# Kernel optimization log

Hardware: AMD Instinct MI355X
Metric: run time of the kernel (lower is better)

The kernel has to match this reference:

```python
import jax, jax.numpy as jnp
import numpy as np

K = 50          # NEC paper uses p=50 neighbors
DELTA = 1e-3    # kernel smoothing constant


def setup_inputs() -> dict:
    key = jax.random.key(0)
    ks = jax.random.split(key, 8)
    B, D_IN, D, A, C = 512, 2, 128, 3, 200000
    s = lambda fan_in: 1.0 / np.sqrt(fan_in)
    return {
        "x": jax.random.normal(ks[0], (B, D_IN), jnp.float32),
        "W1": jax.random.normal(ks[1], (D_IN, D), jnp.float32) * s(D_IN),
        "b1": jnp.zeros((D,), jnp.float32),
        "W2": jax.random.normal(ks[2], (D, D), jnp.float32) * s(D),
        "b2": jnp.zeros((D,), jnp.float32),
        "W3": jax.random.normal(ks[3], (D, D), jnp.float32) * s(D),
        "b3": jnp.zeros((D,), jnp.float32),
        "W4": jax.random.normal(ks[4], (D, D), jnp.float32) * s(D),
        "b4": jnp.zeros((D,), jnp.float32),
        "keys": jax.random.normal(ks[5], (A, C, D), jnp.float32),
        "mem_values": jax.random.normal(ks[6], (A, C), jnp.float32),
    }


def _encode(x, W1, b1, W2, b2, W3, b3, W4, b4):
    h = jax.nn.relu(x @ W1 + b1)
    h = jax.nn.relu(h @ W2 + b2)
    h = jax.nn.relu(h @ W3 + b3)
    return h @ W4 + b4  # [B, D]


def _dnd_lookup(h, keys, mem_values):
    # h: [B, D]; keys: [A, C, D]; mem_values: [A, C]
    q2 = jnp.sum(h * h, axis=-1)                       # [B]
    k2 = jnp.sum(keys * keys, axis=-1)                 # [A, C]
    cross = jnp.einsum("bd,acd->bac", h, keys)         # [B, A, C]
    d2 = jnp.maximum(q2[:, None, None] + k2[None] - 2.0 * cross, 0.0)
    neg_d, idx = jax.lax.top_k(-d2, K)                  # [B, A, K]
    d_top = -neg_d
    w = 1.0 / (d_top + DELTA)                           # NEC kernel
    w = w / jnp.sum(w, axis=-1, keepdims=True)
    a_idx = jnp.arange(keys.shape[0])[None, :, None]    # [1, A, 1]
    v_top = mem_values[a_idx, idx]                      # gather -> [B, A, K]
    values = jnp.sum(w * v_top, axis=-1)                # [B, A]
    return values


def reference(x, W1, b1, W2, b2, W3, b3, W4, b4, keys, mem_values):
    h = _encode(x, W1, b1, W2, b2, W3, b3, W4, b4)
    values = _dnd_lookup(h, keys, mem_values)
    actions = jnp.argmax(values, axis=-1)
    return values, actions
```

## Files before the change

### kernel.cpp

```cpp
#include <hip/hip_runtime.h>
#include <hip/hip_bf16.h>
#include <math.h>

#define B_    512
#define DIM   128
#define A_    3
#define C_    200000
#define K_    50
#define DELTA 1e-3

typedef __attribute__((ext_vector_type(8))) short bf16x8;
typedef __attribute__((ext_vector_type(4))) float f32x4;

#define NBIN_A 128
#define CAP_A  1024
#define ROWCH  12500

#define NSEG3  32
#define TPS3   98
#define NT3    3125

#define AOFF_H64   0u
#define AOFF_H32   524288u
#define AOFF_HBF   786432u
#define AOFF_Q2    917504u
#define AOFF_V64   1718272u
#define AOFF_BINS  8022016u
#define NEED_A     (8022016ull + 307200000ull)

#define NBIN_B 192
#define CAP_B  768
#define BM_B   64
#define BN_B   128
#define TPC_B  16
#define CHUNK_B (TPC_B*BN_B)
#define NCH_B  ((C_ + CHUNK_B - 1)/CHUNK_B)

#define BOFF_H32   0u
#define BOFF_H64   262144u
#define BOFF_Q2    786432u
#define BOFF_K2    788480u
#define BOFF_HIST  3188480u
#define BOFF_TAU   4368128u
#define BOFF_CNT   4374272u
#define BOFF_V64   4380416u
#define BOFF_CAND  4392704u

static __device__ inline unsigned short f2bf(float x) {
    union { float f; unsigned u; } c; c.f = x;
    unsigned r = (c.u + 0x7FFFu + ((c.u >> 16) & 1u)) >> 16;
    return (unsigned short)r;
}
static __device__ inline unsigned pkbf(float a, float b) {
    __hip_bfloat162 t = __float22bfloat162_rn(make_float2(a, b));
    union { __hip_bfloat162 h; unsigned u; } cv; cv.h = t; return cv.u;
}

__global__ __launch_bounds__(128) void mlp_kernel(
    const float* __restrict__ x,
    const float* __restrict__ W1, const float* __restrict__ b1,
    const float* __restrict__ W2, const float* __restrict__ b2,
    const float* __restrict__ W3, const float* __restrict__ b3,
    const float* __restrict__ W4, const float* __restrict__ b4,
    float* __restrict__ h32, unsigned short* __restrict__ hbf,
    double* __restrict__ h64, float* __restrict__ q2)
{
    int b = blockIdx.x, t = threadIdx.x;
    __shared__ double s0[DIM], s1[DIM];
    double x0 = (double)x[b*2+0], x1 = (double)x[b*2+1];
    double h = x0*(double)W1[t] + x1*(double)W1[DIM+t] + (double)b1[t];
    s0[t] = h > 0.0 ? h : 0.0;
    __syncthreads();
    double acc = (double)b2[t];
    for (int k = 0; k < DIM; k++) acc += s0[k]*(double)W2[k*DIM+t];
    s1[t] = acc > 0.0 ? acc : 0.0;
    __syncthreads();
    acc = (double)b3[t];
    for (int k = 0; k < DIM; k++) acc += s1[k]*(double)W3[k*DIM+t];
    s0[t] = acc > 0.0 ? acc : 0.0;
    __syncthreads();
    acc = (double)b4[t];
    for (int k = 0; k < DIM; k++) acc += s0[k]*(double)W4[k*DIM+t];
    h64[b*DIM+t] = acc;
    float hf = (float)acc;
    h32[b*DIM+t] = hf;
    hbf[b*DIM+t] = f2bf(hf);
    s1[t] = acc*acc;
    __syncthreads();
    for (int s = 64; s > 0; s >>= 1) { if (t < s) s1[t] += s1[t+s]; __syncthreads(); }
    if (t == 0) q2[b] = (float)s1[0];
}

static __device__ inline void load4(float4 lv[4], const float* __restrict__ ka,
                                    int nrow, int hh) {
    const float4* gp = (const float4*)(ka + (size_t)nrow*DIM) + hh*4;
    #pragma unroll
    for (int qq = 0; qq < 4; qq++) lv[qq] = gp[qq];
}
static __device__ inline void conv_store(const float4 lv[4], char* sBn,
                                         float* k2n, int r, int hh) {
    float ss = 0.f;
    int4 pk0, pk1;
    {
        float4 v0 = lv[0], v1 = lv[1];
        ss += v0.x*v0.x + v0.y*v0.y + v0.z*v0.z + v0.w*v0.w
            + v1.x*v1.x + v1.y*v1.y + v1.z*v1.z + v1.w*v1.w;
        pk0.x = (int)pkbf(v0.x, v0.y); pk0.y = (int)pkbf(v0.z, v0.w);
        pk0.z = (int)pkbf(v1.x, v1.y); pk0.w = (int)pkbf(v1.z, v1.w);
    }
    {
        float4 v0 = lv[2], v1 = lv[3];
        ss += v0.x*v0.x + v0.y*v0.y + v0.z*v0.z + v0.w*v0.w
            + v1.x*v1.x + v1.y*v1.y + v1.z*v1.z + v1.w*v1.w;
        pk1.x = (int)pkbf(v0.x, v0.y); pk1.y = (int)pkbf(v0.z, v0.w);
        pk1.z = (int)pkbf(v1.x, v1.y); pk1.w = (int)pkbf(v1.z, v1.w);
    }
    char* base = sBn + r*256;
    *(int4*)(base + (((hh*2    ) ^ (r & 7)) << 4)) = pk0;
    *(int4*)(base + (((hh*2 + 1) ^ (r & 7)) << 4)) = pk1;
    ss += __shfl_xor(ss, 1, 64);
    ss += __shfl_xor(ss, 2, 64);
    ss += __shfl_xor(ss, 4, 64);
    if (hh == 0) k2n[r] = ss;
}

__global__ __launch_bounds__(512, 6) void gemm3_kernel(
    const float* __restrict__ keys, const unsigned short* __restrict__ hbf,
    const float* __restrict__ q2, unsigned char* __restrict__ bins)
{
    const int seg = blockIdx.x, my = blockIdx.y, a = blockIdx.z;
    const int b0 = my*64;
    const int tid = threadIdx.x;
    const int lane = tid & 63, w = tid >> 6;
    const int lm = lane & 15, kh = lane >> 4;
    const int wn = w & 1, wm = w >> 1;

    const int tbeg = seg*TPS3;
    int tcnt = NT3 - tbeg;
    if (tcnt <= 0) return;
    if (tcnt > TPS3) tcnt = TPS3;

    __shared__ __align__(16) short sA[8192];
    __shared__ __align__(16) short sB[2][8192];
    __shared__ float q2s[64];
    __shared__ float k2s[2][64];

    {
        #pragma unroll
        for (int u = 0; u < 2; u++) {
            int idx = tid*2 + u;
            int rr = idx >> 4, cc = idx & 15;
            const int4 gv = ((const int4*)hbf)[(size_t)(b0 + rr)*16 + cc];
            *(int4*)((char*)sA + rr*256 + ((cc ^ (rr & 7)) << 4)) = gv;
        }
        if (tid < 64) q2s[tid] = q2[b0 + tid];
    }

    const int r = tid >> 3, hh = tid & 7;
    const float* ka = keys + (size_t)a*C_*DIM;

    float4 lv[4];
    load4(lv, ka, tbeg*64 + r, hh);
    conv_store(lv, (char*)&sB[0][0], k2s[0], r, hh);
    __syncthreads();

    unsigned char* bp_base = bins + ((size_t)(a*B_ + b0))*C_;
    const int bcol = wm*16 + lm;
    const size_t soff0 = (size_t)bcol*C_ + (wn*32 + 0*16 + kh*4);
    const size_t soff1 = (size_t)bcol*C_ + (wn*32 + 1*16 + kh*4);

    unsigned pk_prev0 = 0, pk_prev1 = 0;
    int n0_prev = 0;

    int cur = 0;
    for (int t = 0; t < tcnt; t++) {
        const int n0 = (tbeg + t)*64;
        const bool more = (t + 1 < tcnt);

        if (more) load4(lv, ka, n0 + 64 + r, hh);
        if (t > 0) {
            *(unsigned*)(bp_base + n0_prev + soff0) = pk_prev0;
            *(unsigned*)(bp_base + n0_prev + soff1) = pk_prev1;
        }

        f32x4 acc[2];
        acc[0] = (f32x4){0.f, 0.f, 0.f, 0.f};
        acc[1] = (f32x4){0.f, 0.f, 0.f, 0.f};

        const char* sBc = (const char*)&sB[cur][0];
        #pragma unroll
        for (int kst = 0; kst < 4; kst++) {
            bf16x8 af[2], bfv;
            #pragma unroll
            for (int i = 0; i < 2; i++) {
                int nr = wn*32 + i*16 + lm;
                af[i] = *(const bf16x8*)(sBc + nr*256 + ((((kst<<2) + kh) ^ (nr & 7)) << 4));
            }
            {
                int br = wm*16 + lm;
                bfv = *(const bf16x8*)((const char*)sA + br*256 + ((((kst<<2) + kh) ^ (br & 7)) << 4));
            }
            #pragma unroll
            for (int i = 0; i < 2; i++)
                acc[i] = __builtin_amdgcn_mfma_f32_16x16x32_bf16(af[i], bfv, acc[i], 0, 0, 0);
        }

        {
            const float q2v = q2s[bcol];
            #pragma unroll
            for (int i = 0; i < 2; i++) {
                int nl = wn*32 + i*16 + kh*4;
                float4 kq = *(const float4*)&k2s[cur][nl];
                unsigned pk = 0;
                #pragma unroll
                for (int rg = 0; rg < 4; rg++) {
                    float kv = (rg == 0) ? kq.x : (rg == 1) ? kq.y : (rg == 2) ? kq.z : kq.w;
                    float d2v = (q2v + kv) - 2.0f*acc[i][rg];
                    float dc = fminf(fmaxf(d2v, 16.0f), 4095.0f);
                    unsigned bin = (__float_as_uint(dc) >> 19) - 2096u;
                    pk |= bin << (8*rg);
                }
                if (i == 0) pk_prev0 = pk; else pk_prev1 = pk;
            }
            n0_prev = n0;
        }

        if (more) conv_store(lv, (char*)&sB[cur ^ 1][0], k2s[cur ^ 1], r, hh);
        __syncthreads();
        cur ^= 1;
    }
    *(unsigned*)(bp_base + n0_prev + soff0) = pk_prev0;
    *(unsigned*)(bp_base + n0_prev + soff1) = pk_prev1;
}

__global__ __launch_bounds__(512) void finish_kernel(
    const unsigned char* __restrict__ bins, const float* __restrict__ keys,
    const double* __restrict__ h64, const float* __restrict__ mem_values,
    float* __restrict__ out_values, double* __restrict__ val64)
{
    const int q = blockIdx.x;
    const int a = q >> 9, b = q & 511;
    const int p = b*A_ + a;
    const int tid = threadIdx.x;

    __shared__ unsigned hist_s[NBIN_A*32];
    __shared__ unsigned hc[NBIN_A];
    __shared__ double hd[DIM];
    __shared__ int    cidx[CAP_A];
    __shared__ double d2s[CAP_A];
    __shared__ float  vs[CAP_A];
    __shared__ double redv[8];
    __shared__ int    redi8[8];
    __shared__ double acc_w, acc_wv;
    __shared__ unsigned cnt_s;
    __shared__ int thr_s;

    for (int i = tid; i < NBIN_A*32; i += 512) hist_s[i] = 0;
    for (int i = tid; i < DIM; i += 512) hd[i] = h64[(size_t)b*DIM + i];
    if (tid == 0) { cnt_s = 0; acc_w = 0.0; acc_wv = 0.0; }
    __syncthreads();

    const uint4* row = (const uint4*)(bins + (size_t)q*C_);
    const int rep = tid & 31;
    for (int ch = tid; ch < ROWCH; ch += 512) {
        uint4 v = row[ch];
        unsigned d[4] = {v.x, v.y, v.z, v.w};
        #pragma unroll
        for (int e = 0; e < 4; e++) {
            unsigned x = d[e];
            atomicAdd(&hist_s[((x      ) & 127u)*32 + rep], 1u);
            atomicAdd(&hist_s[((x >>  8) & 127u)*32 + rep], 1u);
            atomicAdd(&hist_s[((x >> 16) & 127u)*32 + rep], 1u);
            atomicAdd(&hist_s[((x >> 24) & 127u)*32 + rep], 1u);
        }
    }
    __syncthreads();
    if (tid < NBIN_A) {
        unsigned s = 0;
        #pragma unroll
        for (int r2 = 0; r2 < 32; r2++) s += hist_s[tid*32 + r2];
        hc[tid] = s;
    }
    __syncthreads();
    if (tid == 0) {
        unsigned cum = 0; int jsel = NBIN_A-1;
        for (int j = 0; j < NBIN_A; j++) { cum += hc[j]; if (cum >= K_) { jsel = j; break; } }
        unsigned c1 = cum + (jsel+1 < NBIN_A ? hc[jsel+1] : 0u);
        unsigned c2 = c1  + (jsel+2 < NBIN_A ? hc[jsel+2] : 0u);
        int jt = (c2 <= 768u) ? jsel+2 : jsel+1;
        if (jt > NBIN_A-1) jt = NBIN_A-1;
        thr_s = jt + 1;
    }
    __syncthreads();
    const unsigned thr  = (unsigned)thr_s;
    const unsigned addv = (128u - thr) * 0x01010101u;
    for (int ch = tid; ch < ROWCH; ch += 512) {
        uint4 v = row[ch];
        unsigned d[4] = {v.x, v.y, v.z, v.w};
        #pragma unroll
        for (int e = 0; e < 4; e++) {
            unsigned m = (d[e] + addv) & 0x80808080u;
            if (m != 0x80808080u) {
                #pragma unroll
                for (int by = 0; by < 4; by++) {
                    if (!((m >> (8*by + 7)) & 1u)) {
                        unsigned pos = atomicAdd(&cnt_s, 1u);
                        if (pos < CAP_A) cidx[pos] = ch*16 + e*4 + by;
                    }
                }
            }
        }
    }
    __syncthreads();
    int n = (int)cnt_s; if (n > CAP_A) n = CAP_A;

    for (int i = tid; i < n; i += 512) {
        int c = cidx[i];
        const float4* kr = (const float4*)(keys + ((size_t)a*C_ + c)*DIM);
        double s0 = 0.0, s1 = 0.0;
        #pragma unroll 4
        for (int kq = 0; kq < 32; kq++) {
            float4 kv = kr[kq];
            double d0 = hd[4*kq+0] - (double)kv.x;
            double d1 = hd[4*kq+1] - (double)kv.y;
            double d2 = hd[4*kq+2] - (double)kv.z;
            double d3 = hd[4*kq+3] - (double)kv.w;
            s0 += d0*d0 + d1*d1; s1 += d2*d2 + d3*d3;
        }
        d2s[i] = s0 + s1;
        vs[i]  = mem_values[(size_t)a*C_ + c];
    }
    __syncthreads();

    int kk = n < K_ ? n : K_;
    for (int t = 0; t < kk; t++) {
        double best = 1e300; int bi = -1;
        for (int i = tid; i < n; i += 512)
            if (d2s[i] < best) { best = d2s[i]; bi = i; }
        #pragma unroll
        for (int off = 32; off > 0; off >>= 1) {
            double ov = __shfl_xor(best, off, 64);
            int    oi = __shfl_xor(bi,   off, 64);
            if (ov < best) { best = ov; bi = oi; }
        }
        int wv = tid >> 6;
        if ((tid & 63) == 0) { redv[wv] = best; redi8[wv] = bi; }
        __syncthreads();
        if (tid == 0) {
            double bv = redv[0]; int wi = redi8[0];
            #pragma unroll
            for (int u = 1; u < 8; u++)
                if (redv[u] < bv) { bv = redv[u]; wi = redi8[u]; }
            double d = d2s[wi]; if (d < 0.0) d = 0.0;
            double wgt = 1.0 / (d + DELTA);
            acc_w += wgt; acc_wv += wgt * (double)vs[wi];
            d2s[wi] = 2e300;
        }
        __syncthreads();
    }
    if (tid == 0) {
        double v = acc_wv / acc_w;
        out_values[p] = (float)v;
        val64[p] = v;
    }
}

__global__ __launch_bounds__(256) void k2_kernel(const float* __restrict__ keys,
                                                 float* __restrict__ k2)
{
    int r = blockIdx.x*4 + (threadIdx.x >> 6);
    int lane = threadIdx.x & 63;
    float2 v = ((const float2*)keys)[(size_t)r*64 + lane];
    float s = v.x*v.x + v.y*v.y;
    #pragma unroll
    for (int off = 32; off > 0; off >>= 1) s += __shfl_down(s, off, 64);
    if (lane == 0) k2[r] = s;
}

template<int MODE>
__global__ __launch_bounds__(256) void pass_kernel(
    const float* __restrict__ keys, const float* __restrict__ h32,
    const float* __restrict__ q2,   const float* __restrict__ k2,
    unsigned* __restrict__ hist,    const float* __restrict__ tau,
    unsigned* __restrict__ cnt,     int* __restrict__ cand)
{
    const int bt = blockIdx.x;
    const int ch = blockIdx.y;
    const int a  = blockIdx.z;
    const int b0 = bt*BM_B;
    const int tid = threadIdx.x;
    const int tx = tid & 31, ty = tid >> 5;

    __shared__ float4 hs4[BM_B*33];
    __shared__ float4 ks4[BN_B*33];
    __shared__ float  q2s[BM_B];
    __shared__ float  taus[BM_B];
    __shared__ unsigned hist_s[MODE == 0 ? BM_B*NBIN_B : 1];

    #pragma unroll
    for (int q = 0; q < BM_B*32/256; q++) {
        int flat = q*256 + tid; int row = flat >> 5, kq = flat & 31;
        hs4[row*33 + kq] = ((const float4*)h32)[(size_t)(b0+row)*32 + kq];
    }
    if (tid < BM_B) {
        q2s[tid] = q2[b0+tid];
        if (MODE == 1) taus[tid] = tau[(b0+tid)*A_ + a];
    }
    if (MODE == 0) for (int i = tid; i < BM_B*NBIN_B; i += 256) hist_s[i] = 0;
    const float* __restrict__ k2g = k2 + (size_t)a*C_;

    for (int t = 0; t < TPC_B; t++) {
        int n0 = ch*CHUNK_B + t*BN_B;
        if (n0 >= C_) break;
        __syncthreads();
        #pragma unroll
        for (int q = 0; q < 16; q++) {
            int flat = q*256 + tid; int row = flat >> 5, kq = flat & 31;
            int nr = n0 + row; if (nr >= C_) nr = C_-1;
            ks4[row*33 + kq] = ((const float4*)keys)[((size_t)a*C_ + nr)*32 + kq];
        }
        __syncthreads();

        float acc[8][4];
        #pragma unroll
        for (int i = 0; i < 8; i++)
            #pragma unroll
            for (int j = 0; j < 4; j++) acc[i][j] = 0.0f;

        for (int kq = 0; kq < 32; kq++) {
            float4 hv[8], kv[4];
            #pragma unroll
            for (int i = 0; i < 8; i++) hv[i] = hs4[(ty*8+i)*33 + kq];
            #pragma unroll
            for (int j = 0; j < 4; j++) kv[j] = ks4[(j*32+tx)*33 + kq];
            #pragma unroll
            for (int i = 0; i < 8; i++)
                #pragma unroll
                for (int j = 0; j < 4; j++)
                    acc[i][j] += hv[i].x*kv[j].x + hv[i].y*kv[j].y
                               + hv[i].z*kv[j].z + hv[i].w*kv[j].w;
        }

        #pragma unroll
        for (int i = 0; i < 8; i++) {
            int bl = ty*8 + i;
            float q2b = q2s[bl];
            #pragma unroll
            for (int j = 0; j < 4; j++) {
                int n = n0 + j*32 + tx;
                if (n < C_) {
                    float d2f = fmaxf(q2b + k2g[n] - 2.0f*acc[i][j], 0.0f);
                    if (MODE == 0) {
                        int bin = (int)(__float_as_uint(d2f + 1.0f) >> 19) - 2032;
                        bin = bin < 0 ? 0 : (bin > NBIN_B-1 ? NBIN_B-1 : bin);
                        atomicAdd(&hist_s[bl*NBIN_B + bin], 1u);
                    } else {
                        if (d2f < taus[bl]) {
                            int p = (b0+bl)*A_ + a;
                            unsigned pos = atomicAdd(&cnt[p], 1u);
                            if (pos < CAP_B) cand[(size_t)p*CAP_B + pos] = n;
                        }
                    }
                }
            }
        }
    }
    if (MODE == 0) {
        __syncthreads();
        for (int i = tid; i < BM_B*NBIN_B; i += 256) {
            unsigned v = hist_s[i];
            if (v) {
                int bl = i / NBIN_B, bin = i % NBIN_B;
                atomicAdd(&hist[(size_t)((b0+bl)*A_ + a)*NBIN_B + bin], v);
            }
        }
    }
}

__global__ __launch_bounds__(256) void tauB_kernel(const unsigned* __restrict__ hist,
                                                   float* __restrict__ tau)
{
    int p = blockIdx.x*256 + threadIdx.x;
    if (p >= B_*A_) return;
    const unsigned* hp = hist + (size_t)p*NBIN_B;
    unsigned cum = 0; int jsel = NBIN_B-1;
    for (int j = 0; j < NBIN_B; j++) { cum += hp[j]; if (cum >= K_) { jsel = j; break; } }
    tau[p] = __uint_as_float((unsigned)(2034 + jsel) << 19) - 1.0f;
}

__global__ __launch_bounds__(256) void select_kernel(
    const float* __restrict__ keys, const double* __restrict__ h64,
    const float* __restrict__ mem_values,
    const unsigned* __restrict__ cnt, const int* __restrict__ cand,
    float* __restrict__ out_values, double* __restrict__ val64, int cap)
{
    int p = blockIdx.x; int b = p / A_, a = p % A_;
    int tid = threadIdx.x;
    __shared__ double hd[DIM];
    __shared__ double d2s[CAP_A];
    __shared__ float  vs[CAP_A];
    __shared__ double redv[4];
    __shared__ int    redi4[4];
    __shared__ double acc_w, acc_wv;

    for (int i = tid; i < DIM; i += 256) hd[i] = h64[(size_t)b*DIM + i];
    if (tid == 0) { acc_w = 0.0; acc_wv = 0.0; }
    __syncthreads();

    int n = (int)cnt[p]; if (n > cap) n = cap;
    for (int i = tid; i < n; i += 256) {
        int c = cand[(size_t)p*cap + i];
        const float4* kr = (const float4*)(keys + ((size_t)a*C_ + c)*DIM);
        double s0 = 0.0, s1 = 0.0;
        #pragma unroll 4
        for (int kq = 0; kq < 32; kq++) {
            float4 kv = kr[kq];
            double d0 = hd[4*kq+0] - (double)kv.x;
            double d1 = hd[4*kq+1] - (double)kv.y;
            double d2 = hd[4*kq+2] - (double)kv.z;
            double d3 = hd[4*kq+3] - (double)kv.w;
            s0 += d0*d0 + d1*d1; s1 += d2*d2 + d3*d3;
        }
        d2s[i] = s0 + s1;
        vs[i]  = mem_values[(size_t)a*C_ + c];
    }
    __syncthreads();

    int kk = n < K_ ? n : K_;
    for (int t = 0; t < kk; t++) {
        double best = 1e300; int bi = -1;
        for (int i = tid; i < n; i += 256)
            if (d2s[i] < best) { best = d2s[i]; bi = i; }
        #pragma unroll
        for (int off = 32; off > 0; off >>= 1) {
            double ov = __shfl_xor(best, off, 64);
            int    oi = __shfl_xor(bi,   off, 64);
            if (ov < best) { best = ov; bi = oi; }
        }
        int wv = tid >> 6;
        if ((tid & 63) == 0) { redv[wv] = best; redi4[wv] = bi; }
        __syncthreads();
        if (tid == 0) {
            double bv = redv[0]; int wi = redi4[0];
            if (redv[1] < bv) { bv = redv[1]; wi = redi4[1]; }
            if (redv[2] < bv) { bv = redv[2]; wi = redi4[2]; }
            if (redv[3] < bv) { bv = redv[3]; wi = redi4[3]; }
            double d = d2s[wi]; if (d < 0.0) d = 0.0;
            double wgt = 1.0 / (d + DELTA);
            acc_w += wgt; acc_wv += wgt * (double)vs[wi];
            d2s[wi] = 2e300;
        }
        __syncthreads();
    }
    if (tid == 0) {
        double v = acc_wv / acc_w;
        out_values[p] = (float)v;
        val64[p] = v;
    }
}

__global__ void argmax_kernel(const double* __restrict__ val64, float* __restrict__ out)
{
    int b = blockIdx.x*blockDim.x + threadIdx.x;
    if (b >= B_) return;
    double v0 = val64[b*A_+0], v1 = val64[b*A_+1], v2 = val64[b*A_+2];
    int bi = 0; double bv = v0;
    if (v1 > bv) { bv = v1; bi = 1; }
    if (v2 > bv) { bv = v2; bi = 2; }
    out[B_*A_ + b] = (float)bi;
}

extern "C" void kernel_launch(void* const* d_in, const int* in_sizes, int n_in,
                              void* d_out, int out_size, void* d_ws, size_t ws_size,
                              hipStream_t stream)
{
    const float* x    = (const float*)d_in[0];
    const float* W1   = (const float*)d_in[1];
    const float* b1   = (const float*)d_in[2];
    const float* W2   = (const float*)d_in[3];
    const float* b2   = (const float*)d_in[4];
    const float* W3   = (const float*)d_in[5];
    const float* b3   = (const float*)d_in[6];
    const float* W4   = (const float*)d_in[7];
    const float* b4   = (const float*)d_in[8];
    const float* keys = (const float*)d_in[9];
    const float* memv = (const float*)d_in[10];

    char* ws = (char*)d_ws;

    if (ws_size >= NEED_A) {
        double*         h64  = (double*)        (ws + AOFF_H64);
        float*          h32  = (float*)         (ws + AOFF_H32);
        unsigned short* hbf  = (unsigned short*)(ws + AOFF_HBF);
        float*          q2   = (float*)         (ws + AOFF_Q2);
        double*         v64  = (double*)        (ws + AOFF_V64);
        unsigned char*  bins = (unsigned char*) (ws + AOFF_BINS);

        mlp_kernel<<<B_, 128, 0, stream>>>(x, W1, b1, W2, b2, W3, b3, W4, b4, h32, hbf, h64, q2);
        gemm3_kernel<<<dim3(NSEG3, 8, A_), 512, 0, stream>>>(keys, hbf, q2, bins);
        finish_kernel<<<B_*A_, 512, 0, stream>>>(bins, keys, h64, memv, (float*)d_out, v64);
        argmax_kernel<<<2, 256, 0, stream>>>(v64, (float*)d_out);
    } else {
        float*          h32  = (float*)         (ws + BOFF_H32);
        double*         h64  = (double*)        (ws + BOFF_H64);
        float*          q2   = (float*)         (ws + BOFF_Q2);
        float*          k2   = (float*)         (ws + BOFF_K2);
        unsigned*       hist = (unsigned*)      (ws + BOFF_HIST);
        float*          tau  = (float*)         (ws + BOFF_TAU);
        unsigned*       cnt  = (unsigned*)      (ws + BOFF_CNT);
        double*         v64  = (double*)        (ws + BOFF_V64);
        int*            cand = (int*)           (ws + BOFF_CAND);
        unsigned short* hbf  = (unsigned short*)(ws + BOFF_CAND);

        hipMemsetAsync(ws + BOFF_HIST, 0, (BOFF_CNT + B_*A_*4) - BOFF_HIST, stream);

        mlp_kernel<<<B_, 128, 0, stream>>>(x, W1, b1, W2, b2, W3, b3, W4, b4, h32, hbf, h64, q2);
        k2_kernel<<<(A_*C_)/4, 256, 0, stream>>>(keys, k2);
        pass_kernel<0><<<dim3(B_/BM_B, NCH_B, A_), 256, 0, stream>>>(keys, h32, q2, k2, hist, nullptr, nullptr, nullptr);
        tauB_kernel<<<(B_*A_ + 255)/256, 256, 0, stream>>>(hist, tau);
        pass_kernel<1><<<dim3(B_/BM_B, NCH_B, A_), 256, 0, stream>>>(keys, h32, q2, k2, nullptr, tau, cnt, cand);
        select_kernel<<<B_*A_, 256, 0, stream>>>(keys, h64, memv, cnt, cand, (float*)d_out, v64, CAP_B);
        argmax_kernel<<<2, 256, 0, stream>>>(v64, (float*)d_out);
    }
}
```

Before: 1.085 ms.

## Keep all queries resident in LDS so each key tile is read once

```diff
diff --git a/kernel.cpp b/kernel.cpp
--- a/kernel.cpp
+++ b/kernel.cpp
@@ -16,9 +16,9 @@
 #define CAP_A  1024
 #define ROWCH  12500
 
-#define NSEG3  32
-#define TPS3   98
-#define NT3    3125
+#define NBLK4  250
+#define GT4    32
+#define GTPB4  25
 
 #define AOFF_H64   0u
 #define AOFF_H32   524288u
@@ -91,146 +91,153 @@
     if (t == 0) q2[b] = (float)s1[0];
 }
 
-static __device__ inline void load4(float4 lv[4], const float* __restrict__ ka,
+static __device__ inline void load2(float4 lv[2], const float* __restrict__ ka,
                                     int nrow, int hh) {
-    const float4* gp = (const float4*)(ka + (size_t)nrow*DIM) + hh*4;
-    #pragma unroll
-    for (int qq = 0; qq < 4; qq++) lv[qq] = gp[qq];
-}
-static __device__ inline void conv_store(const float4 lv[4], char* sBn,
-                                         float* k2n, int r, int hh) {
-    float ss = 0.f;
-    int4 pk0, pk1;
-    {
-        float4 v0 = lv[0], v1 = lv[1];
-        ss += v0.x*v0.x + v0.y*v0.y + v0.z*v0.z + v0.w*v0.w
-            + v1.x*v1.x + v1.y*v1.y + v1.z*v1.z + v1.w*v1.w;
-        pk0.x = (int)pkbf(v0.x, v0.y); pk0.y = (int)pkbf(v0.z, v0.w);
-        pk0.z = (int)pkbf(v1.x, v1.y); pk0.w = (int)pkbf(v1.z, v1.w);
-    }
-    {
-        float4 v0 = lv[2], v1 = lv[3];
-        ss += v0.x*v0.x + v0.y*v0.y + v0.z*v0.z + v0.w*v0.w
-            + v1.x*v1.x + v1.y*v1.y + v1.z*v1.z + v1.w*v1.w;
-        pk1.x = (int)pkbf(v0.x, v0.y); pk1.y = (int)pkbf(v0.z, v0.w);
-        pk1.z = (int)pkbf(v1.x, v1.y); pk1.w = (int)pkbf(v1.z, v1.w);
-    }
-    char* base = sBn + r*256;
-    *(int4*)(base + (((hh*2    ) ^ (r & 7)) << 4)) = pk0;
-    *(int4*)(base + (((hh*2 + 1) ^ (r & 7)) << 4)) = pk1;
+    const float4* gp = (const float4*)(ka + (size_t)nrow*DIM) + hh*2;
+    lv[0] = gp[0]; lv[1] = gp[1];
+}
+static __device__ inline void conv_store32(const float4 lv[2], char* sBn,
+                                           float* k2n, int r, int hh) {
+    float4 v0 = lv[0], v1 = lv[1];
+    float ss = v0.x*v0.x + v0.y*v0.y + v0.z*v0.z + v0.w*v0.w
+             + v1.x*v1.x + v1.y*v1.y + v1.z*v1.z + v1.w*v1.w;
+    int4 pk;
+    pk.x = (int)pkbf(v0.x, v0.y); pk.y = (int)pkbf(v0.z, v0.w);
+    pk.z = (int)pkbf(v1.x, v1.y); pk.w = (int)pkbf(v1.z, v1.w);
+    *(int4*)(sBn + r*256 + ((hh ^ (r & 7)) << 4)) = pk;
     ss += __shfl_xor(ss, 1, 64);
     ss += __shfl_xor(ss, 2, 64);
     ss += __shfl_xor(ss, 4, 64);
+    ss += __shfl_xor(ss, 8, 64);
     if (hh == 0) k2n[r] = ss;
 }
 
-__global__ __launch_bounds__(512, 6) void gemm3_kernel(
+__global__ __launch_bounds__(512, 1) void gemm4_kernel(
     const float* __restrict__ keys, const unsigned short* __restrict__ hbf,
     const float* __restrict__ q2, unsigned char* __restrict__ bins)
 {
-    const int seg = blockIdx.x, my = blockIdx.y, a = blockIdx.z;
-    const int b0 = my*64;
+    const int blk = blockIdx.x, a = blockIdx.y;
     const int tid = threadIdx.x;
     const int lane = tid & 63, w = tid >> 6;
     const int lm = lane & 15, kh = lane >> 4;
-    const int wn = w & 1, wm = w >> 1;
-
-    const int tbeg = seg*TPS3;
-    int tcnt = NT3 - tbeg;
-    if (tcnt <= 0) return;
-    if (tcnt > TPS3) tcnt = TPS3;
-
-    __shared__ __align__(16) short sA[8192];
-    __shared__ __align__(16) short sB[2][8192];
-    __shared__ float q2s[64];
-    __shared__ float k2s[2][64];
-
+
+    __shared__ __align__(16) short sA[512*128];
+    __shared__ __align__(16) short sB[2][32*128];
+    __shared__ float q2s[512];
+    __shared__ float k2s[2][32];
+
+    #pragma unroll
+    for (int u = 0; u < 16; u++) {
+        int idx = u*512 + tid;
+        int rr = idx >> 4, cc = idx & 15;
+        int4 gv = ((const int4*)hbf)[rr*16 + cc];
+        *(int4*)((char*)sA + rr*256 + ((cc ^ (rr & 7)) << 4)) = gv;
+    }
+    q2s[tid] = q2[tid];
+
+    const int r = tid >> 4, hh = tid & 15;
+    const float* ka = keys + (size_t)a*C_*DIM;
+    const int nbase = blk*(GT4*GTPB4);
+
+    float4 lv[2];
+    load2(lv, ka, nbase + r, hh);
+    conv_store32(lv, (char*)&sB[0][0], k2s[0], r, hh);
+    __syncthreads();
+
+    unsigned char* rp0; unsigned char* rp1; unsigned char* rp2; unsigned char* rp3;
     {
-        #pragma unroll
-        for (int u = 0; u < 2; u++) {
-            int idx = tid*2 + u;
-            int rr = idx >> 4, cc = idx & 15;
-            const int4 gv = ((const int4*)hbf)[(size_t)(b0 + rr)*16 + cc];
-            *(int4*)((char*)sA + rr*256 + ((cc ^ (rr & 7)) << 4)) = gv;
-        }
-        if (tid < 64) q2s[tid] = q2[b0 + tid];
-    }
-
-    const int r = tid >> 3, hh = tid & 7;
-    const float* ka = keys + (size_t)a*C_*DIM;
-
-    float4 lv[4];
-    load4(lv, ka, tbeg*64 + r, hh);
-    conv_store(lv, (char*)&sB[0][0], k2s[0], r, hh);
-    __syncthreads();
-
-    unsigned char* bp_base = bins + ((size_t)(a*B_ + b0))*C_;
-    const int bcol = wm*16 + lm;
-    const size_t soff0 = (size_t)bcol*C_ + (wn*32 + 0*16 + kh*4);
-    const size_t soff1 = (size_t)bcol*C_ + (wn*32 + 1*16 + kh*4);
-
-    unsigned pk_prev0 = 0, pk_prev1 = 0;
+        unsigned char* base = bins + (size_t)(a*B_)*C_ + kh*4;
+        rp0 = base + (size_t)(w*64 +  0 + lm)*C_;
+        rp1 = base + (size_t)(w*64 + 16 + lm)*C_;
+        rp2 = base + (size_t)(w*64 + 32 + lm)*C_;
+        rp3 = base + (size_t)(w*64 + 48 + lm)*C_;
+    }
+
+    unsigned pkp[8];
+    #pragma unroll
+    for (int u = 0; u < 8; u++) pkp[u] = 0;
     int n0_prev = 0;
 
     int cur = 0;
-    for (int t = 0; t < tcnt; t++) {
-        const int n0 = (tbeg + t)*64;
-        const bool more = (t + 1 < tcnt);
-
-        if (more) load4(lv, ka, n0 + 64 + r, hh);
+    for (int t = 0; t < GTPB4; t++) {
+        const int n0 = nbase + t*GT4;
+        const bool more = (t + 1 < GTPB4);
+
+        if (more) load2(lv, ka, n0 + GT4 + r, hh);
         if (t > 0) {
-            *(unsigned*)(bp_base + n0_prev + soff0) = pk_prev0;
-            *(unsigned*)(bp_base + n0_prev + soff1) = pk_prev1;
-        }
-
-        f32x4 acc[2];
-        acc[0] = (f32x4){0.f, 0.f, 0.f, 0.f};
-        acc[1] = (f32x4){0.f, 0.f, 0.f, 0.f};
+            *(unsigned*)(rp0 + n0_prev     ) = pkp[0];
+            *(unsigned*)(rp0 + n0_prev + 16) = pkp[1];
+            *(unsigned*)(rp1 + n0_prev     ) = pkp[2];
+            *(unsigned*)(rp1 + n0_prev + 16) = pkp[3];
+            *(unsigned*)(rp2 + n0_prev     ) = pkp[4];
+            *(unsigned*)(rp2 + n0_prev + 16) = pkp[5];
+            *(unsigned*)(rp3 + n0_prev     ) = pkp[6];
+            *(unsigned*)(rp3 + n0_prev + 16) = pkp[7];
+        }
+
+        f32x4 acc[2][4];
+        #pragma unroll
+        for (int i = 0; i < 2; i++)
+            #pragma unroll
+            for (int j = 0; j < 4; j++) acc[i][j] = (f32x4){0.f, 0.f, 0.f, 0.f};
 
         const char* sBc = (const char*)&sB[cur][0];
         #pragma unroll
         for (int kst = 0; kst < 4; kst++) {
-            bf16x8 af[2], bfv;
+            bf16x8 af[2], bfv[4];
             #pragma unroll
             for (int i = 0; i < 2; i++) {
-                int nr = wn*32 + i*16 + lm;
+                int nr = i*16 + lm;
                 af[i] = *(const bf16x8*)(sBc + nr*256 + ((((kst<<2) + kh) ^ (nr & 7)) << 4));
             }
-            {
-                int br = wm*16 + lm;
-                bfv = *(const bf16x8*)((const char*)sA + br*256 + ((((kst<<2) + kh) ^ (br & 7)) << 4));
+            #pragma unroll
+            for (int j = 0; j < 4; j++) {
+                int br = w*64 + j*16 + lm;
+                bfv[j] = *(const bf16x8*)((const char*)sA + br*256 + ((((kst<<2) + kh) ^ (br & 7)) << 4));
             }
             #pragma unroll
             for (int i = 0; i < 2; i++)
-                acc[i] = __builtin_amdgcn_mfma_f32_16x16x32_bf16(af[i], bfv, acc[i], 0, 0, 0);
+                #pragma unroll
+                for (int j = 0; j < 4; j++)
+                    acc[i][j] = __builtin_amdgcn_mfma_f32_16x16x32_bf16(af[i], bfv[j], acc[i][j], 0, 0, 0);
         }
 
         {
-            const float q2v = q2s[bcol];
-            #pragma unroll
-            for (int i = 0; i < 2; i++) {
-                int nl = wn*32 + i*16 + kh*4;
-                float4 kq = *(const float4*)&k2s[cur][nl];
-                unsigned pk = 0;
+            float4 kq0 = *(const float4*)&k2s[cur][kh*4];
+            float4 kq1 = *(const float4*)&k2s[cur][16 + kh*4];
+            #pragma unroll
+            for (int j = 0; j < 4; j++) {
+                float q2v = q2s[w*64 + j*16 + lm];
                 #pragma unroll
-                for (int rg = 0; rg < 4; rg++) {
-                    float kv = (rg == 0) ? kq.x : (rg == 1) ? kq.y : (rg == 2) ? kq.z : kq.w;
-                    float d2v = (q2v + kv) - 2.0f*acc[i][rg];
-                    float dc = fminf(fmaxf(d2v, 16.0f), 4095.0f);
-                    unsigned bin = (__float_as_uint(dc) >> 19) - 2096u;
-                    pk |= bin << (8*rg);
+                for (int i = 0; i < 2; i++) {
+                    float4 kq = (i == 0) ? kq0 : kq1;
+                    unsigned pk = 0;
+                    #pragma unroll
+                    for (int rg = 0; rg < 4; rg++) {
+                        float kv = (rg == 0) ? kq.x : (rg == 1) ? kq.y : (rg == 2) ? kq.z : kq.w;
+                        float d2v = (q2v + kv) - 2.0f*acc[i][j][rg];
+                        float dc = fminf(fmaxf(d2v, 16.0f), 4095.0f);
+                        unsigned bin = (__float_as_uint(dc) >> 19) - 2096u;
+                        pk |= bin << (8*rg);
+                    }
+                    pkp[j*2 + i] = pk;
                 }
-                if (i == 0) pk_prev0 = pk; else pk_prev1 = pk;
             }
             n0_prev = n0;
         }
 
-        if (more) conv_store(lv, (char*)&sB[cur ^ 1][0], k2s[cur ^ 1], r, hh);
+        if (more) conv_store32(lv, (char*)&sB[cur ^ 1][0], k2s[cur ^ 1], r, hh);
         __syncthreads();
         cur ^= 1;
     }
-    *(unsigned*)(bp_base + n0_prev + soff0) = pk_prev0;
-    *(unsigned*)(bp_base + n0_prev + soff1) = pk_prev1;
+    *(unsigned*)(rp0 + n0_prev     ) = pkp[0];
+    *(unsigned*)(rp0 + n0_prev + 16) = pkp[1];
+    *(unsigned*)(rp1 + n0_prev     ) = pkp[2];
+    *(unsigned*)(rp1 + n0_prev + 16) = pkp[3];
+    *(unsigned*)(rp2 + n0_prev     ) = pkp[4];
+    *(unsigned*)(rp2 + n0_prev + 16) = pkp[5];
+    *(unsigned*)(rp3 + n0_prev     ) = pkp[6];
+    *(unsigned*)(rp3 + n0_prev + 16) = pkp[7];
 }
 
 __global__ __launch_bounds__(512) void finish_kernel(
@@ -597,7 +604,7 @@
         unsigned char*  bins = (unsigned char*) (ws + AOFF_BINS);
 
         mlp_kernel<<<B_, 128, 0, stream>>>(x, W1, b1, W2, b2, W3, b3, W4, b4, h32, hbf, h64, q2);
-        gemm3_kernel<<<dim3(NSEG3, 8, A_), 512, 0, stream>>>(keys, hbf, q2, bins);
+        gemm4_kernel<<<dim3(NBLK4, A_), 512, 0, stream>>>(keys, hbf, q2, bins);
         finish_kernel<<<B_*A_, 512, 0, stream>>>(bins, keys, h64, memv, (float*)d_out, v64);
         argmax_kernel<<<2, 256, 0, stream>>>(v64, (float*)d_out);
     } else {
```

New measurement: 966.6 us. -10.9%, faster.
